# Kernel optimization log

Hardware: AMD Instinct MI355X
Metric: run time of the kernel (lower is better)

The kernel has to match this reference:

```python
import jax, jax.numpy as jnp
import numpy as np

ALPHA_BASE = 1.2
ALPHA_SCALE = 0.3
GRAPH_LAMBDA = 0.3
FUSION_BETA = 0.1
PRIOR_BETA = 0.2
LN_EPS = 1e-5  # nn.LayerNorm default

B, L, C = 8, 8192, 512
STAT, HID, GF, EMB = 4, 16, 16, 16


def _linear_params(key, out_d, in_d):
    kw, kb = jax.random.split(key)
    bound = 1.0 / np.sqrt(in_d)
    W = jax.random.uniform(kw, (out_d, in_d), minval=-bound, maxval=bound, dtype=jnp.float32)
    b = jax.random.uniform(kb, (out_d,), minval=-bound, maxval=bound, dtype=jnp.float32)
    return W, b


def setup_inputs() -> dict:
    key = jax.random.key(0)
    ks = jax.random.split(key, 9)
    residual = jax.random.normal(ks[0], (B, L, C), dtype=jnp.float32)
    node_embedding = jax.random.normal(ks[1], (C, EMB), dtype=jnp.float32) * 0.02
    W_l1, b_l1 = _linear_params(ks[2], HID, STAT)
    W_l2, b_l2 = _linear_params(ks[3], HID, HID)
    W_g, b_g = _linear_params(ks[4], HID, STAT)
    W_q, b_q = _linear_params(ks[5], GF, STAT)
    W_k, b_k = _linear_params(ks[6], GF, STAT)
    W_f, b_f = _linear_params(ks[7], HID, HID)
    W_o, b_o = _linear_params(ks[8], 1, HID)
    ln_g = jnp.ones((HID,), jnp.float32)
    ln_b = jnp.zeros((HID,), jnp.float32)
    return dict(residual=residual, node_embedding=node_embedding,
                W_l1=W_l1, b_l1=b_l1, W_l2=W_l2, b_l2=b_l2,
                W_g=W_g, b_g=b_g, W_q=W_q, b_q=b_q, W_k=W_k, b_k=b_k,
                W_f=W_f, b_f=b_f, W_o=W_o, b_o=b_o, ln_g=ln_g, ln_b=ln_b)


def reference(residual, node_embedding, W_l1, b_l1, W_l2, b_l2, W_g, b_g,
              W_q, b_q, W_k, b_k, W_f, b_f, W_o, b_o, ln_g, ln_b):
    # --- residual statistics: [B,L,C] -> [B,C,4] ---
    abs_res = jnp.abs(residual)
    m = abs_res.mean(axis=1)                       # mean(|r|)
    mx = abs_res.max(axis=1)                       # max(|r|)
    sq = (residual * residual).mean(axis=1)        # energy == mean(|r|^2)
    std = jnp.sqrt(jnp.maximum(sq - m * m, 0.0))   # biased std of |r|
    h0 = jnp.stack([m, mx, std, sq], axis=-1)      # [B,C,4]

    # --- local branch ---
    h_local = jax.nn.relu(h0 @ W_l1.T + b_l1) @ W_l2.T + b_l2  # [B,C,H]

    # --- adaptive adjacency ---
    q = h0 @ W_q.T + b_q                            # [B,C,G]
    k = h0 @ W_k.T + b_k                            # [B,C,G]
    sim_data = jax.nn.relu(jnp.einsum('bcg,bdg->bcd', q, k))
    sim_prior = jax.nn.relu(node_embedding @ node_embedding.T)  # [C,C]
    eye = jnp.eye(sim_data.shape[-1], dtype=sim_data.dtype)
    sim = sim_data + PRIOR_BETA * sim_prior[None] + eye[None]
    A = jax.nn.softmax(sim, axis=-1)                # [B,C,C]

    # --- message passing ---
    h_graph_in = h0 @ W_g.T + b_g                   # [B,C,H]
    msg = jnp.einsum('bcd,bdh->bch', A, h_graph_in)
    h_graph = h_graph_in + GRAPH_LAMBDA * jax.nn.relu(msg)

    # --- fusion + layernorm + head ---
    h = h_local + FUSION_BETA * h_graph
    mu = h.mean(axis=-1, keepdims=True)
    var = ((h - mu) ** 2).mean(axis=-1, keepdims=True)
    h = (h - mu) / jnp.sqrt(var + LN_EPS) * ln_g + ln_b
    h = jax.nn.relu(h @ W_f.T + b_f)
    delta = ALPHA_SCALE * jnp.tanh(h @ W_o.T + b_o)  # [B,C,1]
    alpha = (ALPHA_BASE + delta).transpose(0, 2, 1)  # [B,1,C]
    return alpha, h0, A
```

## Files before the change

### kernel.cpp

```cpp
#include <hip/hip_runtime.h>
#include <math.h>

#define BB 8
#define LL 8192
#define CC 512
#define NCHUNK 256

#define H0_OFF (BB*CC)
#define A_OFF  (H0_OFF + BB*CC*4)

#define F_ALPHA_BASE 1.2f
#define F_ALPHA_SCALE 0.3f
#define F_GRAPH_LAMBDA 0.3f
#define F_FUSION_BETA 0.1f
#define F_PRIOR_BETA 0.2f
#define F_LN_EPS 1e-5f

__global__ __launch_bounds__(256) void k_stats(const float* __restrict__ res,
                                               float* __restrict__ pbuf) {
    __shared__ float comb[3][CC];
    int b = blockIdx.x >> 8;
    int cb = blockIdx.x & 255;
    int sub = threadIdx.x >> 7;
    int c4 = (threadIdx.x & 127) * 4;
    const float* base = res + ((size_t)b * LL + (size_t)cb * 32 + sub * 16) * CC + c4;

    float s0 = 0.f, s1 = 0.f, s2 = 0.f, s3 = 0.f;
    float m0 = 0.f, m1 = 0.f, m2 = 0.f, m3 = 0.f;
    float q0 = 0.f, q1 = 0.f, q2 = 0.f, q3 = 0.f;
    #pragma unroll
    for (int r = 0; r < 16; r++) {
        float4 v = *(const float4*)(base + (size_t)r * CC);
        s0 += fabsf(v.x); s1 += fabsf(v.y); s2 += fabsf(v.z); s3 += fabsf(v.w);
        m0 = fmaxf(m0, fabsf(v.x)); m1 = fmaxf(m1, fabsf(v.y));
        m2 = fmaxf(m2, fabsf(v.z)); m3 = fmaxf(m3, fabsf(v.w));
        q0 = fmaf(v.x, v.x, q0); q1 = fmaf(v.y, v.y, q1);
        q2 = fmaf(v.z, v.z, q2); q3 = fmaf(v.w, v.w, q3);
    }
    if (sub == 1) {
        *(float4*)&comb[0][c4] = make_float4(s0, s1, s2, s3);
        *(float4*)&comb[1][c4] = make_float4(m0, m1, m2, m3);
        *(float4*)&comb[2][c4] = make_float4(q0, q1, q2, q3);
    }
    __syncthreads();
    if (sub == 0) {
        float4 cs = *(const float4*)&comb[0][c4];
        float4 cm = *(const float4*)&comb[1][c4];
        float4 cq = *(const float4*)&comb[2][c4];
        s0 += cs.x; s1 += cs.y; s2 += cs.z; s3 += cs.w;
        m0 = fmaxf(m0, cm.x); m1 = fmaxf(m1, cm.y);
        m2 = fmaxf(m2, cm.z); m3 = fmaxf(m3, cm.w);
        q0 += cq.x; q1 += cq.y; q2 += cq.z; q3 += cq.w;
        float* pb = pbuf + ((size_t)(b * 3) * NCHUNK + cb) * CC + c4;
        *(float4*)(pb)                        = make_float4(s0, s1, s2, s3);
        *(float4*)(pb + (size_t)NCHUNK * CC)     = make_float4(m0, m1, m2, m3);
        *(float4*)(pb + (size_t)2 * NCHUNK * CC) = make_float4(q0, q1, q2, q3);
    }
}

__global__ __launch_bounds__(256) void k_red(const float* __restrict__ pbuf,
                                             float* __restrict__ out) {
    __shared__ float red[4][3][16];
    int b = blockIdx.x >> 5;
    int c16g = blockIdx.x & 31;
    int coff = threadIdx.x & 15;
    int part = threadIdx.x >> 4;
    int c = c16g * 16 + coff;

    const float* pA = pbuf + ((size_t)(b * 3 + 0) * NCHUNK + part * 16) * CC + c;
    const float* pB = pbuf + ((size_t)(b * 3 + 1) * NCHUNK + part * 16) * CC + c;
    const float* pC = pbuf + ((size_t)(b * 3 + 2) * NCHUNK + part * 16) * CC + c;
    float sum = 0.f, mx = 0.f, sq = 0.f;
    #pragma unroll
    for (int i = 0; i < 16; i++) {
        sum += pA[(size_t)i * CC];
        mx = fmaxf(mx, pB[(size_t)i * CC]);
        sq += pC[(size_t)i * CC];
    }
    sum += __shfl_xor(sum, 16); sum += __shfl_xor(sum, 32);
    mx = fmaxf(mx, __shfl_xor(mx, 16)); mx = fmaxf(mx, __shfl_xor(mx, 32));
    sq += __shfl_xor(sq, 16); sq += __shfl_xor(sq, 32);
    int w = threadIdx.x >> 6;
    if ((threadIdx.x & 63) < 16) {
        red[w][0][coff] = sum;
        red[w][1][coff] = mx;
        red[w][2][coff] = sq;
    }
    __syncthreads();
    if (threadIdx.x < 16) {
        float ts = red[0][0][coff] + red[1][0][coff] + red[2][0][coff] + red[3][0][coff];
        float tm = fmaxf(fmaxf(red[0][1][coff], red[1][1][coff]),
                         fmaxf(red[2][1][coff], red[3][1][coff]));
        float tq = red[0][2][coff] + red[1][2][coff] + red[2][2][coff] + red[3][2][coff];
        float m = ts * (1.f / LL);
        float sqm = tq * (1.f / LL);
        float sd = sqrtf(fmaxf(sqm - m * m, 0.f));
        int g = b * CC + c16g * 16 + coff;
        *(float4*)(out + H0_OFF + (size_t)g * 4) = make_float4(m, tm, sd, sqm);
    }
}

__global__ __launch_bounds__(256) void k_rows(
    const float* __restrict__ h0,
    const float* __restrict__ ne,
    const float* __restrict__ Wl1, const float* __restrict__ bl1,
    const float* __restrict__ Wl2, const float* __restrict__ bl2,
    const float* __restrict__ Wg,  const float* __restrict__ bg,
    const float* __restrict__ Wq,  const float* __restrict__ bq,
    const float* __restrict__ Wk,  const float* __restrict__ bk,
    const float* __restrict__ Wf,  const float* __restrict__ bf,
    const float* __restrict__ Wo,  const float* __restrict__ bo,
    const float* __restrict__ lng, const float* __restrict__ lnb,
    float* __restrict__ out) {
    __shared__ float kls[8 * CC * 2];
    __shared__ float hgls[8 * CC * 2];
    int b = blockIdx.x >> 6;
    int rb = blockIdx.x & 63;
    int wid = threadIdx.x >> 6;
    int lane = threadIdx.x & 63;
    int row0 = rb * 8 + wid * 2;

    float nr[2][16];
    #pragma unroll
    for (int rr = 0; rr < 2; rr++) {
        #pragma unroll
        for (int t = 0; t < 4; t++) {
            float4 v = *(const float4*)(ne + (size_t)(row0 + rr) * 16 + t * 4);
            nr[rr][4 * t] = v.x; nr[rr][4 * t + 1] = v.y;
            nr[rr][4 * t + 2] = v.z; nr[rr][4 * t + 3] = v.w;
        }
    }
    float pr[2][8];
    #pragma unroll
    for (int j = 0; j < 8; j++) {
        int col = lane + 64 * j;
        float d0 = 0.f, d1 = 0.f;
        #pragma unroll
        for (int t = 0; t < 4; t++) {
            float4 v = *(const float4*)(ne + (size_t)col * 16 + t * 4);
            d0 = fmaf(nr[0][4 * t], v.x, d0); d0 = fmaf(nr[0][4 * t + 1], v.y, d0);
            d0 = fmaf(nr[0][4 * t + 2], v.z, d0); d0 = fmaf(nr[0][4 * t + 3], v.w, d0);
            d1 = fmaf(nr[1][4 * t], v.x, d1); d1 = fmaf(nr[1][4 * t + 1], v.y, d1);
            d1 = fmaf(nr[1][4 * t + 2], v.z, d1); d1 = fmaf(nr[1][4 * t + 3], v.w, d1);
        }
        pr[0][j] = fmaxf(d0, 0.f);
        pr[1][j] = fmaxf(d1, 0.f);
    }

    #pragma unroll
    for (int ccy = 0; ccy < 2; ccy++) {
        int col = threadIdx.x + ccy * 256;
        float4 hv = *(const float4*)(h0 + ((size_t)b * CC + col) * 4);
        float s[4] = {hv.x, hv.y, hv.z, hv.w};
        #pragma unroll
        for (int t2 = 0; t2 < 8; t2++) {
            float k0 = bk[2 * t2], k1 = bk[2 * t2 + 1];
            float g0 = bg[2 * t2], g1 = bg[2 * t2 + 1];
            #pragma unroll
            for (int j = 0; j < 4; j++) {
                k0 = fmaf(Wk[(2 * t2) * 4 + j], s[j], k0);
                k1 = fmaf(Wk[(2 * t2 + 1) * 4 + j], s[j], k1);
                g0 = fmaf(Wg[(2 * t2) * 4 + j], s[j], g0);
                g1 = fmaf(Wg[(2 * t2 + 1) * 4 + j], s[j], g1);
            }
            *(float2*)&kls[(t2 * CC + col) * 2] = make_float2(k0, k1);
            *(float2*)&hgls[(t2 * CC + col) * 2] = make_float2(g0, g1);
        }
    }
    __syncthreads();

    float s2[2][4];
    float qr[2][16];
    #pragma unroll
    for (int rr = 0; rr < 2; rr++) {
        float4 hr = *(const float4*)(h0 + ((size_t)b * CC + row0 + rr) * 4);
        s2[rr][0] = hr.x; s2[rr][1] = hr.y; s2[rr][2] = hr.z; s2[rr][3] = hr.w;
        #pragma unroll
        for (int i = 0; i < 16; i++) {
            float a = bq[i];
            #pragma unroll
            for (int j = 0; j < 4; j++) a = fmaf(Wq[i * 4 + j], s2[rr][j], a);
            qr[rr][i] = a;
        }
    }

    float sv[2][8];
    float mx0 = -1e30f, mx1 = -1e30f;
    #pragma unroll
    for (int j = 0; j < 8; j++) {
        int col = lane + 64 * j;
        float a0 = 0.f, a1 = 0.f;
        #pragma unroll
        for (int t2 = 0; t2 < 8; t2++) {
            float2 kk = *(const float2*)&kls[(t2 * CC + col) * 2];
            a0 = fmaf(qr[0][2 * t2], kk.x, a0);
            a0 = fmaf(qr[0][2 * t2 + 1], kk.y, a0);
            a1 = fmaf(qr[1][2 * t2], kk.x, a1);
            a1 = fmaf(qr[1][2 * t2 + 1], kk.y, a1);
        }
        float v0 = fmaxf(a0, 0.f) + F_PRIOR_BETA * pr[0][j] + (col == row0 ? 1.f : 0.f);
        float v1 = fmaxf(a1, 0.f) + F_PRIOR_BETA * pr[1][j] + (col == row0 + 1 ? 1.f : 0.f);
        sv[0][j] = v0; sv[1][j] = v1;
        mx0 = fmaxf(mx0, v0); mx1 = fmaxf(mx1, v1);
    }
    #pragma unroll
    for (int o = 32; o; o >>= 1) {
        mx0 = fmaxf(mx0, __shfl_xor(mx0, o));
        mx1 = fmaxf(mx1, __shfl_xor(mx1, o));
    }

    float ls0 = 0.f, ls1 = 0.f;
    float msg[2][16];
    #pragma unroll
    for (int h = 0; h < 16; h++) { msg[0][h] = 0.f; msg[1][h] = 0.f; }
    #pragma unroll
    for (int j = 0; j < 8; j++) {
        int col = lane + 64 * j;
        float e0 = expf(sv[0][j] - mx0);
        float e1 = expf(sv[1][j] - mx1);
        sv[0][j] = e0; sv[1][j] = e1;
        ls0 += e0; ls1 += e1;
        #pragma unroll
        for (int t2 = 0; t2 < 8; t2++) {
            float2 hh = *(const float2*)&hgls[(t2 * CC + col) * 2];
            msg[0][2 * t2]     = fmaf(e0, hh.x, msg[0][2 * t2]);
            msg[0][2 * t2 + 1] = fmaf(e0, hh.y, msg[0][2 * t2 + 1]);
            msg[1][2 * t2]     = fmaf(e1, hh.x, msg[1][2 * t2]);
            msg[1][2 * t2 + 1] = fmaf(e1, hh.y, msg[1][2 * t2 + 1]);
        }
    }
    #pragma unroll
    for (int o = 32; o; o >>= 1) {
        ls0 += __shfl_xor(ls0, o);
        ls1 += __shfl_xor(ls1, o);
    }
    float inv0 = 1.f / ls0, inv1 = 1.f / ls1;

    float* arow0 = out + A_OFF + ((size_t)b * CC + row0) * CC;
    #pragma unroll
    for (int j = 0; j < 8; j++) {
        arow0[lane + 64 * j]      = sv[0][j] * inv0;
        arow0[CC + lane + 64 * j] = sv[1][j] * inv1;
    }

    #pragma unroll
    for (int h = 0; h < 16; h++) {
        float v0 = msg[0][h], v1 = msg[1][h];
        #pragma unroll
        for (int o = 32; o; o >>= 1) {
            v0 += __shfl_xor(v0, o);
            v1 += __shfl_xor(v1, o);
        }
        msg[0][h] = v0 * inv0;
        msg[1][h] = v1 * inv1;
    }

    #pragma unroll
    for (int rr = 0; rr < 2; rr++) {
        int row = row0 + rr;
        float t1[16];
        #pragma unroll
        for (int i = 0; i < 16; i++) {
            float a = bl1[i];
            #pragma unroll
            for (int j = 0; j < 4; j++) a = fmaf(Wl1[i * 4 + j], s2[rr][j], a);
            t1[i] = fmaxf(a, 0.f);
        }
        float hvec[16];
        float mu = 0.f;
        #pragma unroll
        for (int h = 0; h < 16; h++) {
            float hl = bl2[h];
            #pragma unroll
            for (int j = 0; j < 16; j++) hl = fmaf(Wl2[h * 16 + j], t1[j], hl);
            float hgr = hgls[((h >> 1) * CC + row) * 2 + (h & 1)];
            float hg2 = hgr + F_GRAPH_LAMBDA * fmaxf(msg[rr][h], 0.f);
            float hv = hl + F_FUSION_BETA * hg2;
            hvec[h] = hv;
            mu += hv;
        }
        mu *= (1.f / 16.f);
        float var = 0.f;
        #pragma unroll
        for (int h = 0; h < 16; h++) { float d = hvec[h] - mu; var = fmaf(d, d, var); }
        var *= (1.f / 16.f);
        float istd = 1.f / sqrtf(var + F_LN_EPS);
        float hn[16];
        #pragma unroll
        for (int h = 0; h < 16; h++) hn[h] = (hvec[h] - mu) * istd * lng[h] + lnb[h];

        float acc2 = bo[0];
        #pragma unroll
        for (int o = 0; o < 16; o++) {
            float f = bf[o];
            #pragma unroll
            for (int t = 0; t < 16; t++) f = fmaf(Wf[o * 16 + t], hn[t], f);
            acc2 = fmaf(Wo[o], fmaxf(f, 0.f), acc2);
        }
        float alpha = F_ALPHA_BASE + F_ALPHA_SCALE * tanhf(acc2);
        if (lane == 0) out[(size_t)b * CC + row] = alpha;
    }
}

extern "C" void kernel_launch(void* const* d_in, const int* in_sizes, int n_in,
                              void* d_out, int out_size, void* d_ws, size_t ws_size,
                              hipStream_t stream) {
    const float* res = (const float*)d_in[0];
    const float* ne  = (const float*)d_in[1];
    const float* Wl1 = (const float*)d_in[2];
    const float* bl1 = (const float*)d_in[3];
    const float* Wl2 = (const float*)d_in[4];
    const float* bl2 = (const float*)d_in[5];
    const float* Wg  = (const float*)d_in[6];
    const float* bg  = (const float*)d_in[7];
    const float* Wq  = (const float*)d_in[8];
    const float* bq  = (const float*)d_in[9];
    const float* Wk  = (const float*)d_in[10];
    const float* bk  = (const float*)d_in[11];
    const float* Wf  = (const float*)d_in[12];
    const float* bf  = (const float*)d_in[13];
    const float* Wo  = (const float*)d_in[14];
    const float* bo  = (const float*)d_in[15];
    const float* lng = (const float*)d_in[16];
    const float* lnb = (const float*)d_in[17];
    float* out = (float*)d_out;
    float* pbuf = (float*)d_ws;

    k_stats<<<BB * NCHUNK, 256, 0, stream>>>(res, pbuf);
    k_red<<<BB * 32, 256, 0, stream>>>(pbuf, out);
    k_rows<<<BB * (CC / 8), 256, 0, stream>>>(out + H0_OFF, ne,
                                              Wl1, bl1, Wl2, bl2, Wg, bg, Wq, bq, Wk, bk,
                                              Wf, bf, Wo, bo, lng, lnb, out);
}
```

Baseline: 58.20 us.

## Fuse all phases into one cooperative kernel with algebraic q·k and graph-message shortcuts

Merges the stats, reduction and row kernels into one cooperative kernel separated by grid-wide syncs, falling back to three launches if the cooperative launch fails. The stats phase now uses 512 blocks over larger L chunks instead of 2048 blocks. The prior C×C matrix is precomputed once into workspace instead of per block. The q·k similarity and the message passing are rewritten algebraically: since keys and graph inputs are linear in h0, only a 4-vector per row and 4 weighted sums over columns are needed, which cuts shared memory and FLOPs. The trade-off is the cost of grid syncs and lower parallelism in the streaming stats pass.

```diff
diff --git a/kernel.cpp b/kernel.cpp
--- a/kernel.cpp
+++ b/kernel.cpp
@@ -1,10 +1,13 @@
 #include <hip/hip_runtime.h>
+#include <hip/hip_cooperative_groups.h>
 #include <math.h>
+
+namespace cg = cooperative_groups;
 
 #define BB 8
 #define LL 8192
 #define CC 512
-#define NCHUNK 256
+#define NCH 64
 
 #define H0_OFF (BB*CC)
 #define A_OFF  (H0_OFF + BB*CC*4)
@@ -16,20 +19,25 @@
 #define F_PRIOR_BETA 0.2f
 #define F_LN_EPS 1e-5f
 
-__global__ __launch_bounds__(256) void k_stats(const float* __restrict__ res,
-                                               float* __restrict__ pbuf) {
-    __shared__ float comb[3][CC];
-    int b = blockIdx.x >> 8;
-    int cb = blockIdx.x & 255;
-    int sub = threadIdx.x >> 7;
-    int c4 = (threadIdx.x & 127) * 4;
-    const float* base = res + ((size_t)b * LL + (size_t)cb * 32 + sub * 16) * CC + c4;
-
+struct P {
+    const float* res; const float* ne;
+    const float* Wl1; const float* bl1; const float* Wl2; const float* bl2;
+    const float* Wg;  const float* bg;  const float* Wq;  const float* bq;
+    const float* Wk;  const float* bk;  const float* Wf;  const float* bf;
+    const float* Wo;  const float* bo;  const float* lng; const float* lnb;
+    float* out; float* pbuf; float* prior;
+};
+
+__device__ __forceinline__ void phase_stats(const P& p, float* smem, int blk, int tid) {
+    int b = blk >> 6, cb = blk & 63;
+    int sub = tid >> 7;
+    int c4 = (tid & 127) * 4;
+    const float* base = p.res + ((size_t)b * LL + cb * 128 + sub * 64) * CC + c4;
     float s0 = 0.f, s1 = 0.f, s2 = 0.f, s3 = 0.f;
     float m0 = 0.f, m1 = 0.f, m2 = 0.f, m3 = 0.f;
     float q0 = 0.f, q1 = 0.f, q2 = 0.f, q3 = 0.f;
-    #pragma unroll
-    for (int r = 0; r < 16; r++) {
+    #pragma unroll 8
+    for (int r = 0; r < 64; r++) {
         float4 v = *(const float4*)(base + (size_t)r * CC);
         s0 += fabsf(v.x); s1 += fabsf(v.y); s2 += fabsf(v.z); s3 += fabsf(v.w);
         m0 = fmaxf(m0, fabsf(v.x)); m1 = fmaxf(m1, fabsf(v.y));
@@ -38,168 +46,139 @@
         q2 = fmaf(v.z, v.z, q2); q3 = fmaf(v.w, v.w, q3);
     }
     if (sub == 1) {
-        *(float4*)&comb[0][c4] = make_float4(s0, s1, s2, s3);
-        *(float4*)&comb[1][c4] = make_float4(m0, m1, m2, m3);
-        *(float4*)&comb[2][c4] = make_float4(q0, q1, q2, q3);
+        *(float4*)&smem[0 * CC + c4] = make_float4(s0, s1, s2, s3);
+        *(float4*)&smem[1 * CC + c4] = make_float4(m0, m1, m2, m3);
+        *(float4*)&smem[2 * CC + c4] = make_float4(q0, q1, q2, q3);
     }
     __syncthreads();
     if (sub == 0) {
-        float4 cs = *(const float4*)&comb[0][c4];
-        float4 cm = *(const float4*)&comb[1][c4];
-        float4 cq = *(const float4*)&comb[2][c4];
+        float4 cs = *(const float4*)&smem[0 * CC + c4];
+        float4 cm = *(const float4*)&smem[1 * CC + c4];
+        float4 cq = *(const float4*)&smem[2 * CC + c4];
         s0 += cs.x; s1 += cs.y; s2 += cs.z; s3 += cs.w;
         m0 = fmaxf(m0, cm.x); m1 = fmaxf(m1, cm.y);
         m2 = fmaxf(m2, cm.z); m3 = fmaxf(m3, cm.w);
         q0 += cq.x; q1 += cq.y; q2 += cq.z; q3 += cq.w;
-        float* pb = pbuf + ((size_t)(b * 3) * NCHUNK + cb) * CC + c4;
-        *(float4*)(pb)                        = make_float4(s0, s1, s2, s3);
-        *(float4*)(pb + (size_t)NCHUNK * CC)     = make_float4(m0, m1, m2, m3);
-        *(float4*)(pb + (size_t)2 * NCHUNK * CC) = make_float4(q0, q1, q2, q3);
-    }
-}
-
-__global__ __launch_bounds__(256) void k_red(const float* __restrict__ pbuf,
-                                             float* __restrict__ out) {
-    __shared__ float red[4][3][16];
-    int b = blockIdx.x >> 5;
-    int c16g = blockIdx.x & 31;
-    int coff = threadIdx.x & 15;
-    int part = threadIdx.x >> 4;
-    int c = c16g * 16 + coff;
-
-    const float* pA = pbuf + ((size_t)(b * 3 + 0) * NCHUNK + part * 16) * CC + c;
-    const float* pB = pbuf + ((size_t)(b * 3 + 1) * NCHUNK + part * 16) * CC + c;
-    const float* pC = pbuf + ((size_t)(b * 3 + 2) * NCHUNK + part * 16) * CC + c;
-    float sum = 0.f, mx = 0.f, sq = 0.f;
-    #pragma unroll
-    for (int i = 0; i < 16; i++) {
-        sum += pA[(size_t)i * CC];
-        mx = fmaxf(mx, pB[(size_t)i * CC]);
-        sq += pC[(size_t)i * CC];
-    }
-    sum += __shfl_xor(sum, 16); sum += __shfl_xor(sum, 32);
-    mx = fmaxf(mx, __shfl_xor(mx, 16)); mx = fmaxf(mx, __shfl_xor(mx, 32));
-    sq += __shfl_xor(sq, 16); sq += __shfl_xor(sq, 32);
-    int w = threadIdx.x >> 6;
-    if ((threadIdx.x & 63) < 16) {
-        red[w][0][coff] = sum;
-        red[w][1][coff] = mx;
-        red[w][2][coff] = sq;
+        float* pb = p.pbuf + ((size_t)(b * 3) * NCH + cb) * CC + c4;
+        *(float4*)(pb)                      = make_float4(s0, s1, s2, s3);
+        *(float4*)(pb + (size_t)NCH * CC)     = make_float4(m0, m1, m2, m3);
+        *(float4*)(pb + (size_t)2 * NCH * CC) = make_float4(q0, q1, q2, q3);
+    }
+}
+
+__device__ __forceinline__ void phase_mid(const P& p, float* smem, int blk, int tid) {
+    if (blk < 256) {
+        int b = blk >> 5, c16 = blk & 31;
+        int coff = tid & 15;
+        int part = tid >> 4;
+        int c = c16 * 16 + coff;
+        const float* pA = p.pbuf + ((size_t)(b * 3 + 0) * NCH + part * 4) * CC + c;
+        const float* pB = p.pbuf + ((size_t)(b * 3 + 1) * NCH + part * 4) * CC + c;
+        const float* pC = p.pbuf + ((size_t)(b * 3 + 2) * NCH + part * 4) * CC + c;
+        float sum = 0.f, mx = 0.f, sq = 0.f;
+        #pragma unroll
+        for (int i = 0; i < 4; i++) {
+            sum += pA[(size_t)i * CC];
+            mx = fmaxf(mx, pB[(size_t)i * CC]);
+            sq += pC[(size_t)i * CC];
+        }
+        sum += __shfl_xor(sum, 16); sum += __shfl_xor(sum, 32);
+        mx = fmaxf(mx, __shfl_xor(mx, 16)); mx = fmaxf(mx, __shfl_xor(mx, 32));
+        sq += __shfl_xor(sq, 16); sq += __shfl_xor(sq, 32);
+        int w = tid >> 6;
+        if ((tid & 63) < 16) {
+            smem[(w * 3 + 0) * 16 + coff] = sum;
+            smem[(w * 3 + 1) * 16 + coff] = mx;
+            smem[(w * 3 + 2) * 16 + coff] = sq;
+        }
+        __syncthreads();
+        if (tid < 16) {
+            float ts = smem[0 * 16 + coff] + smem[3 * 16 + coff] + smem[6 * 16 + coff] + smem[9 * 16 + coff];
+            float tm = fmaxf(fmaxf(smem[1 * 16 + coff], smem[4 * 16 + coff]),
+                             fmaxf(smem[7 * 16 + coff], smem[10 * 16 + coff]));
+            float tq = smem[2 * 16 + coff] + smem[5 * 16 + coff] + smem[8 * 16 + coff] + smem[11 * 16 + coff];
+            float m = ts * (1.f / LL);
+            float sqm = tq * (1.f / LL);
+            float sd = sqrtf(fmaxf(sqm - m * m, 0.f));
+            int g = b * CC + c16 * 16 + coff;
+            *(float4*)(p.out + H0_OFF + (size_t)g * 4) = make_float4(m, tm, sd, sqm);
+        }
+    } else {
+        int base_id = (blk - 256) * 1024 + tid;
+        #pragma unroll
+        for (int rep = 0; rep < 4; rep++) {
+            int id = base_id + rep * 256;
+            int c = id >> 9, d = id & 511;
+            const float4* a4 = (const float4*)(p.ne + (size_t)c * 16);
+            const float4* b4 = (const float4*)(p.ne + (size_t)d * 16);
+            float s = 0.f;
+            #pragma unroll
+            for (int t = 0; t < 4; t++) {
+                float4 av = a4[t], bv = b4[t];
+                s = fmaf(av.x, bv.x, s); s = fmaf(av.y, bv.y, s);
+                s = fmaf(av.z, bv.z, s); s = fmaf(av.w, bv.w, s);
+            }
+            p.prior[id] = fmaxf(s, 0.f);
+        }
+    }
+}
+
+__device__ __forceinline__ void phase_rows(const P& p, float* smem, int blk, int tid) {
+    int b = blk >> 6, rb = blk & 63;
+    #pragma unroll
+    for (int ccy = 0; ccy < 2; ccy++) {
+        int col = tid + ccy * 256;
+        float4 hv = *(const float4*)(p.out + H0_OFF + ((size_t)b * CC + col) * 4);
+        smem[col] = hv.x;
+        smem[CC + col] = hv.y;
+        smem[2 * CC + col] = hv.z;
+        smem[3 * CC + col] = hv.w;
     }
     __syncthreads();
-    if (threadIdx.x < 16) {
-        float ts = red[0][0][coff] + red[1][0][coff] + red[2][0][coff] + red[3][0][coff];
-        float tm = fmaxf(fmaxf(red[0][1][coff], red[1][1][coff]),
-                         fmaxf(red[2][1][coff], red[3][1][coff]));
-        float tq = red[0][2][coff] + red[1][2][coff] + red[2][2][coff] + red[3][2][coff];
-        float m = ts * (1.f / LL);
-        float sqm = tq * (1.f / LL);
-        float sd = sqrtf(fmaxf(sqm - m * m, 0.f));
-        int g = b * CC + c16g * 16 + coff;
-        *(float4*)(out + H0_OFF + (size_t)g * 4) = make_float4(m, tm, sd, sqm);
-    }
-}
-
-__global__ __launch_bounds__(256) void k_rows(
-    const float* __restrict__ h0,
-    const float* __restrict__ ne,
-    const float* __restrict__ Wl1, const float* __restrict__ bl1,
-    const float* __restrict__ Wl2, const float* __restrict__ bl2,
-    const float* __restrict__ Wg,  const float* __restrict__ bg,
-    const float* __restrict__ Wq,  const float* __restrict__ bq,
-    const float* __restrict__ Wk,  const float* __restrict__ bk,
-    const float* __restrict__ Wf,  const float* __restrict__ bf,
-    const float* __restrict__ Wo,  const float* __restrict__ bo,
-    const float* __restrict__ lng, const float* __restrict__ lnb,
-    float* __restrict__ out) {
-    __shared__ float kls[8 * CC * 2];
-    __shared__ float hgls[8 * CC * 2];
-    int b = blockIdx.x >> 6;
-    int rb = blockIdx.x & 63;
-    int wid = threadIdx.x >> 6;
-    int lane = threadIdx.x & 63;
+
+    int wid = tid >> 6, lane = tid & 63;
     int row0 = rb * 8 + wid * 2;
 
-    float nr[2][16];
+    float sloc[2][4], u[2][4], c0[2];
     #pragma unroll
     for (int rr = 0; rr < 2; rr++) {
-        #pragma unroll
-        for (int t = 0; t < 4; t++) {
-            float4 v = *(const float4*)(ne + (size_t)(row0 + rr) * 16 + t * 4);
-            nr[rr][4 * t] = v.x; nr[rr][4 * t + 1] = v.y;
-            nr[rr][4 * t + 2] = v.z; nr[rr][4 * t + 3] = v.w;
-        }
-    }
-    float pr[2][8];
+        int row = row0 + rr;
+        float sv0 = smem[row], sv1 = smem[CC + row];
+        float sv2 = smem[2 * CC + row], sv3 = smem[3 * CC + row];
+        sloc[rr][0] = sv0; sloc[rr][1] = sv1; sloc[rr][2] = sv2; sloc[rr][3] = sv3;
+        float uu0 = 0.f, uu1 = 0.f, uu2 = 0.f, uu3 = 0.f, cc = 0.f;
+        #pragma unroll
+        for (int i = 0; i < 16; i++) {
+            float qi = p.bq[i];
+            qi = fmaf(p.Wq[i * 4 + 0], sv0, qi);
+            qi = fmaf(p.Wq[i * 4 + 1], sv1, qi);
+            qi = fmaf(p.Wq[i * 4 + 2], sv2, qi);
+            qi = fmaf(p.Wq[i * 4 + 3], sv3, qi);
+            uu0 = fmaf(qi, p.Wk[i * 4 + 0], uu0);
+            uu1 = fmaf(qi, p.Wk[i * 4 + 1], uu1);
+            uu2 = fmaf(qi, p.Wk[i * 4 + 2], uu2);
+            uu3 = fmaf(qi, p.Wk[i * 4 + 3], uu3);
+            cc = fmaf(qi, p.bk[i], cc);
+        }
+        u[rr][0] = uu0; u[rr][1] = uu1; u[rr][2] = uu2; u[rr][3] = uu3;
+        c0[rr] = cc;
+    }
+
+    const float* prow = p.prior + (size_t)row0 * CC;
+    float sv[2][8];
+    float mx0 = -1e30f, mx1 = -1e30f;
     #pragma unroll
     for (int j = 0; j < 8; j++) {
         int col = lane + 64 * j;
-        float d0 = 0.f, d1 = 0.f;
-        #pragma unroll
-        for (int t = 0; t < 4; t++) {
-            float4 v = *(const float4*)(ne + (size_t)col * 16 + t * 4);
-            d0 = fmaf(nr[0][4 * t], v.x, d0); d0 = fmaf(nr[0][4 * t + 1], v.y, d0);
-            d0 = fmaf(nr[0][4 * t + 2], v.z, d0); d0 = fmaf(nr[0][4 * t + 3], v.w, d0);
-            d1 = fmaf(nr[1][4 * t], v.x, d1); d1 = fmaf(nr[1][4 * t + 1], v.y, d1);
-            d1 = fmaf(nr[1][4 * t + 2], v.z, d1); d1 = fmaf(nr[1][4 * t + 3], v.w, d1);
-        }
-        pr[0][j] = fmaxf(d0, 0.f);
-        pr[1][j] = fmaxf(d1, 0.f);
-    }
-
-    #pragma unroll
-    for (int ccy = 0; ccy < 2; ccy++) {
-        int col = threadIdx.x + ccy * 256;
-        float4 hv = *(const float4*)(h0 + ((size_t)b * CC + col) * 4);
-        float s[4] = {hv.x, hv.y, hv.z, hv.w};
-        #pragma unroll
-        for (int t2 = 0; t2 < 8; t2++) {
-            float k0 = bk[2 * t2], k1 = bk[2 * t2 + 1];
-            float g0 = bg[2 * t2], g1 = bg[2 * t2 + 1];
-            #pragma unroll
-            for (int j = 0; j < 4; j++) {
-                k0 = fmaf(Wk[(2 * t2) * 4 + j], s[j], k0);
-                k1 = fmaf(Wk[(2 * t2 + 1) * 4 + j], s[j], k1);
-                g0 = fmaf(Wg[(2 * t2) * 4 + j], s[j], g0);
-                g1 = fmaf(Wg[(2 * t2 + 1) * 4 + j], s[j], g1);
-            }
-            *(float2*)&kls[(t2 * CC + col) * 2] = make_float2(k0, k1);
-            *(float2*)&hgls[(t2 * CC + col) * 2] = make_float2(g0, g1);
-        }
-    }
-    __syncthreads();
-
-    float s2[2][4];
-    float qr[2][16];
-    #pragma unroll
-    for (int rr = 0; rr < 2; rr++) {
-        float4 hr = *(const float4*)(h0 + ((size_t)b * CC + row0 + rr) * 4);
-        s2[rr][0] = hr.x; s2[rr][1] = hr.y; s2[rr][2] = hr.z; s2[rr][3] = hr.w;
-        #pragma unroll
-        for (int i = 0; i < 16; i++) {
-            float a = bq[i];
-            #pragma unroll
-            for (int j = 0; j < 4; j++) a = fmaf(Wq[i * 4 + j], s2[rr][j], a);
-            qr[rr][i] = a;
-        }
-    }
-
-    float sv[2][8];
-    float mx0 = -1e30f, mx1 = -1e30f;
-    #pragma unroll
-    for (int j = 0; j < 8; j++) {
-        int col = lane + 64 * j;
-        float a0 = 0.f, a1 = 0.f;
-        #pragma unroll
-        for (int t2 = 0; t2 < 8; t2++) {
-            float2 kk = *(const float2*)&kls[(t2 * CC + col) * 2];
-            a0 = fmaf(qr[0][2 * t2], kk.x, a0);
-            a0 = fmaf(qr[0][2 * t2 + 1], kk.y, a0);
-            a1 = fmaf(qr[1][2 * t2], kk.x, a1);
-            a1 = fmaf(qr[1][2 * t2 + 1], kk.y, a1);
-        }
-        float v0 = fmaxf(a0, 0.f) + F_PRIOR_BETA * pr[0][j] + (col == row0 ? 1.f : 0.f);
-        float v1 = fmaxf(a1, 0.f) + F_PRIOR_BETA * pr[1][j] + (col == row0 + 1 ? 1.f : 0.f);
+        float h0c = smem[col], h1c = smem[CC + col];
+        float h2c = smem[2 * CC + col], h3c = smem[3 * CC + col];
+        float d0 = c0[0], d1 = c0[1];
+        d0 = fmaf(u[0][0], h0c, d0); d1 = fmaf(u[1][0], h0c, d1);
+        d0 = fmaf(u[0][1], h1c, d0); d1 = fmaf(u[1][1], h1c, d1);
+        d0 = fmaf(u[0][2], h2c, d0); d1 = fmaf(u[1][2], h2c, d1);
+        d0 = fmaf(u[0][3], h3c, d0); d1 = fmaf(u[1][3], h3c, d1);
+        float v0 = fmaxf(d0, 0.f) + F_PRIOR_BETA * prow[col] + (col == row0 ? 1.f : 0.f);
+        float v1 = fmaxf(d1, 0.f) + F_PRIOR_BETA * prow[CC + col] + (col == row0 + 1 ? 1.f : 0.f);
         sv[0][j] = v0; sv[1][j] = v1;
         mx0 = fmaxf(mx0, v0); mx1 = fmaxf(mx1, v1);
     }
@@ -210,9 +189,7 @@
     }
 
     float ls0 = 0.f, ls1 = 0.f;
-    float msg[2][16];
-    #pragma unroll
-    for (int h = 0; h < 16; h++) { msg[0][h] = 0.f; msg[1][h] = 0.f; }
+    float T0[4] = {0.f, 0.f, 0.f, 0.f}, T1[4] = {0.f, 0.f, 0.f, 0.f};
     #pragma unroll
     for (int j = 0; j < 8; j++) {
         int col = lane + 64 * j;
@@ -220,62 +197,71 @@
         float e1 = expf(sv[1][j] - mx1);
         sv[0][j] = e0; sv[1][j] = e1;
         ls0 += e0; ls1 += e1;
-        #pragma unroll
-        for (int t2 = 0; t2 < 8; t2++) {
-            float2 hh = *(const float2*)&hgls[(t2 * CC + col) * 2];
-            msg[0][2 * t2]     = fmaf(e0, hh.x, msg[0][2 * t2]);
-            msg[0][2 * t2 + 1] = fmaf(e0, hh.y, msg[0][2 * t2 + 1]);
-            msg[1][2 * t2]     = fmaf(e1, hh.x, msg[1][2 * t2]);
-            msg[1][2 * t2 + 1] = fmaf(e1, hh.y, msg[1][2 * t2 + 1]);
-        }
+        float h0c = smem[col], h1c = smem[CC + col];
+        float h2c = smem[2 * CC + col], h3c = smem[3 * CC + col];
+        T0[0] = fmaf(e0, h0c, T0[0]); T1[0] = fmaf(e1, h0c, T1[0]);
+        T0[1] = fmaf(e0, h1c, T0[1]); T1[1] = fmaf(e1, h1c, T1[1]);
+        T0[2] = fmaf(e0, h2c, T0[2]); T1[2] = fmaf(e1, h2c, T1[2]);
+        T0[3] = fmaf(e0, h3c, T0[3]); T1[3] = fmaf(e1, h3c, T1[3]);
     }
     #pragma unroll
     for (int o = 32; o; o >>= 1) {
-        ls0 += __shfl_xor(ls0, o);
-        ls1 += __shfl_xor(ls1, o);
+        ls0 += __shfl_xor(ls0, o); ls1 += __shfl_xor(ls1, o);
+        T0[0] += __shfl_xor(T0[0], o); T1[0] += __shfl_xor(T1[0], o);
+        T0[1] += __shfl_xor(T0[1], o); T1[1] += __shfl_xor(T1[1], o);
+        T0[2] += __shfl_xor(T0[2], o); T1[2] += __shfl_xor(T1[2], o);
+        T0[3] += __shfl_xor(T0[3], o); T1[3] += __shfl_xor(T1[3], o);
     }
     float inv0 = 1.f / ls0, inv1 = 1.f / ls1;
 
-    float* arow0 = out + A_OFF + ((size_t)b * CC + row0) * CC;
+    float* arow = p.out + A_OFF + ((size_t)b * CC + row0) * CC;
     #pragma unroll
     for (int j = 0; j < 8; j++) {
-        arow0[lane + 64 * j]      = sv[0][j] * inv0;
-        arow0[CC + lane + 64 * j] = sv[1][j] * inv1;
-    }
-
-    #pragma unroll
-    for (int h = 0; h < 16; h++) {
-        float v0 = msg[0][h], v1 = msg[1][h];
-        #pragma unroll
-        for (int o = 32; o; o >>= 1) {
-            v0 += __shfl_xor(v0, o);
-            v1 += __shfl_xor(v1, o);
-        }
-        msg[0][h] = v0 * inv0;
-        msg[1][h] = v1 * inv1;
+        arow[lane + 64 * j]      = sv[0][j] * inv0;
+        arow[CC + lane + 64 * j] = sv[1][j] * inv1;
     }
 
     #pragma unroll
     for (int rr = 0; rr < 2; rr++) {
         int row = row0 + rr;
-        float t1[16];
+        float inv = rr ? inv1 : inv0;
+        float Ta = (rr ? T1[0] : T0[0]) * inv;
+        float Tb = (rr ? T1[1] : T0[1]) * inv;
+        float Tc = (rr ? T1[2] : T0[2]) * inv;
+        float Td = (rr ? T1[3] : T0[3]) * inv;
+        float* s2 = sloc[rr];
+
+        float gcomb[16];
+        #pragma unroll
+        for (int h = 0; h < 16; h++) {
+            float w0 = p.Wg[h * 4 + 0], w1 = p.Wg[h * 4 + 1];
+            float w2 = p.Wg[h * 4 + 2], w3 = p.Wg[h * 4 + 3];
+            float bgh = p.bg[h];
+            float hg = bgh;
+            hg = fmaf(w0, s2[0], hg); hg = fmaf(w1, s2[1], hg);
+            hg = fmaf(w2, s2[2], hg); hg = fmaf(w3, s2[3], hg);
+            float mg = bgh;
+            mg = fmaf(w0, Ta, mg); mg = fmaf(w1, Tb, mg);
+            mg = fmaf(w2, Tc, mg); mg = fmaf(w3, Td, mg);
+            gcomb[h] = hg + F_GRAPH_LAMBDA * fmaxf(mg, 0.f);
+        }
+
+        float t1v[16];
         #pragma unroll
         for (int i = 0; i < 16; i++) {
-            float a = bl1[i];
+            float a = p.bl1[i];
             #pragma unroll
-            for (int j = 0; j < 4; j++) a = fmaf(Wl1[i * 4 + j], s2[rr][j], a);
-            t1[i] = fmaxf(a, 0.f);
+            for (int j = 0; j < 4; j++) a = fmaf(p.Wl1[i * 4 + j], s2[j], a);
+            t1v[i] = fmaxf(a, 0.f);
         }
         float hvec[16];
         float mu = 0.f;
         #pragma unroll
         for (int h = 0; h < 16; h++) {
-            float hl = bl2[h];
+            float hl = p.bl2[h];
             #pragma unroll
-            for (int j = 0; j < 16; j++) hl = fmaf(Wl2[h * 16 + j], t1[j], hl);
-            float hgr = hgls[((h >> 1) * CC + row) * 2 + (h & 1)];
-            float hg2 = hgr + F_GRAPH_LAMBDA * fmaxf(msg[rr][h], 0.f);
-            float hv = hl + F_FUSION_BETA * hg2;
+            for (int j = 0; j < 16; j++) hl = fmaf(p.Wl2[h * 16 + j], t1v[j], hl);
+            float hv = hl + F_FUSION_BETA * gcomb[h];
             hvec[h] = hv;
             mu += hv;
         }
@@ -287,48 +273,76 @@
         float istd = 1.f / sqrtf(var + F_LN_EPS);
         float hn[16];
         #pragma unroll
-        for (int h = 0; h < 16; h++) hn[h] = (hvec[h] - mu) * istd * lng[h] + lnb[h];
-
-        float acc2 = bo[0];
+        for (int h = 0; h < 16; h++) hn[h] = (hvec[h] - mu) * istd * p.lng[h] + p.lnb[h];
+
+        float acc2 = p.bo[0];
         #pragma unroll
         for (int o = 0; o < 16; o++) {
-            float f = bf[o];
+            float f = p.bf[o];
             #pragma unroll
-            for (int t = 0; t < 16; t++) f = fmaf(Wf[o * 16 + t], hn[t], f);
-            acc2 = fmaf(Wo[o], fmaxf(f, 0.f), acc2);
+            for (int t = 0; t < 16; t++) f = fmaf(p.Wf[o * 16 + t], hn[t], f);
+            acc2 = fmaf(p.Wo[o], fmaxf(f, 0.f), acc2);
         }
         float alpha = F_ALPHA_BASE + F_ALPHA_SCALE * tanhf(acc2);
-        if (lane == 0) out[(size_t)b * CC + row] = alpha;
-    }
+        if (lane == 0) p.out[(size_t)b * CC + row] = alpha;
+    }
+}
+
+__global__ __launch_bounds__(256, 4) void k_all(P p) {
+    __shared__ float smem[4 * CC];
+    cg::grid_group grid = cg::this_grid();
+    phase_stats(p, smem, blockIdx.x, threadIdx.x);
+    grid.sync();
+    phase_mid(p, smem, blockIdx.x, threadIdx.x);
+    grid.sync();
+    phase_rows(p, smem, blockIdx.x, threadIdx.x);
+}
+
+__global__ __launch_bounds__(256, 4) void k_p1(P p) {
+    __shared__ float smem[4 * CC];
+    phase_stats(p, smem, blockIdx.x, threadIdx.x);
+}
+__global__ __launch_bounds__(256, 4) void k_p2(P p) {
+    __shared__ float smem[4 * CC];
+    phase_mid(p, smem, blockIdx.x, threadIdx.x);
+}
+__global__ __launch_bounds__(256, 4) void k_p3(P p) {
+    __shared__ float smem[4 * CC];
+    phase_rows(p, smem, blockIdx.x, threadIdx.x);
 }
 
 extern "C" void kernel_launch(void* const* d_in, const int* in_sizes, int n_in,
                               void* d_out, int out_size, void* d_ws, size_t ws_size,
                               hipStream_t stream) {
-    const float* res = (const float*)d_in[0];
-    const float* ne  = (const float*)d_in[1];
-    const float* Wl1 = (const float*)d_in[2];
-    const float* bl1 = (const float*)d_in[3];
-    const float* Wl2 = (const float*)d_in[4];
-    const float* bl2 = (const float*)d_in[5];
-    const float* Wg  = (const float*)d_in[6];
-    const float* bg  = (const float*)d_in[7];
-    const float* Wq  = (const float*)d_in[8];
-    const float* bq  = (const float*)d_in[9];
-    const float* Wk  = (const float*)d_in[10];
-    const float* bk  = (const float*)d_in[11];
-    const float* Wf  = (const float*)d_in[12];
-    const float* bf  = (const float*)d_in[13];
-    const float* Wo  = (const float*)d_in[14];
-    const float* bo  = (const float*)d_in[15];
-    const float* lng = (const float*)d_in[16];
-    const float* lnb = (const float*)d_in[17];
-    float* out = (float*)d_out;
-    float* pbuf = (float*)d_ws;
-
-    k_stats<<<BB * NCHUNK, 256, 0, stream>>>(res, pbuf);
-    k_red<<<BB * 32, 256, 0, stream>>>(pbuf, out);
-    k_rows<<<BB * (CC / 8), 256, 0, stream>>>(out + H0_OFF, ne,
-                                              Wl1, bl1, Wl2, bl2, Wg, bg, Wq, bq, Wk, bk,
-                                              Wf, bf, Wo, bo, lng, lnb, out);
-}
+    P p;
+    p.res = (const float*)d_in[0];
+    p.ne  = (const float*)d_in[1];
+    p.Wl1 = (const float*)d_in[2];
+    p.bl1 = (const float*)d_in[3];
+    p.Wl2 = (const float*)d_in[4];
+    p.bl2 = (const float*)d_in[5];
+    p.Wg  = (const float*)d_in[6];
+    p.bg  = (const float*)d_in[7];
+    p.Wq  = (const float*)d_in[8];
+    p.bq  = (const float*)d_in[9];
+    p.Wk  = (const float*)d_in[10];
+    p.bk  = (const float*)d_in[11];
+    p.Wf  = (const float*)d_in[12];
+    p.bf  = (const float*)d_in[13];
+    p.Wo  = (const float*)d_in[14];
+    p.bo  = (const float*)d_in[15];
+    p.lng = (const float*)d_in[16];
+    p.lnb = (const float*)d_in[17];
+    p.out  = (float*)d_out;
+    p.pbuf = (float*)d_ws;
+    p.prior = (float*)d_ws + (size_t)BB * 3 * NCH * CC;
+
+    void* args[] = { &p };
+    hipError_t err = hipLaunchCooperativeKernel((void*)k_all, dim3(512), dim3(256),
+                                                args, 0, stream);
+    if (err != hipSuccess) {
+        k_p1<<<512, 256, 0, stream>>>(p);
+        k_p2<<<512, 256, 0, stream>>>(p);
+        k_p3<<<512, 256, 0, stream>>>(p);
+    }
+}
```

After: 196.6 us. 3.38x slower.
